# Optimization experiments

Measured on AMD Instinct MI355X. Metric: run time of the kernel, lower is better.

Reference implementation:

```python
import jax, jax.numpy as jnp
import numpy as np

B, A, V, D = 16, 1024, 1024, 512


def setup_inputs() -> dict:
    key = jax.random.key(0)
    k1, k2 = jax.random.split(key)
    audio_encoded = jax.random.normal(k1, (B, A, D), dtype=jnp.float32)
    visual_encoded = jax.random.normal(k2, (B, V, D), dtype=jnp.float32)
    return {"audio_encoded": audio_encoded, "visual_encoded": visual_encoded}


def reference(audio_encoded, visual_encoded):
    # Batched pairwise L2 distance: out[b, a, v] = ||audio[b,a] - visual[b,v]||_2
    # Fused ||a||^2 + ||v||^2 - 2 a.v formulation (single batched GEMM) replacing
    # the original per-(batch, audio-frame) Python loop of diff/pow/sum/sqrt.
    a_sq = jnp.sum(audio_encoded * audio_encoded, axis=-1)   # [B, A]
    v_sq = jnp.sum(visual_encoded * visual_encoded, axis=-1)  # [B, V]
    cross = jnp.einsum("bad,bvd->bav", audio_encoded, visual_encoded)  # [B, A, V]
    dist_sq = a_sq[:, :, None] + v_sq[:, None, :] - 2.0 * cross
    dist_sq = jnp.maximum(dist_sq, 0.0)  # clamp fp round-off negatives
    l2_features = jnp.sqrt(dist_sq)  # [B, A, V]
    return l2_features
```

## Files before the change

### kernel.cpp

```cpp
#include <hip/hip_runtime.h>
#include <hip/hip_bf16.h>

typedef __attribute__((ext_vector_type(8))) short short8;
typedef __attribute__((ext_vector_type(4))) float fv4;

constexpr int B_ = 16, A_ = 1024, V_ = 1024, D_ = 512;

__device__ __forceinline__ unsigned cvtpk(float lo, float hi) {
    unsigned r;
    asm("v_cvt_pk_bf16_f32 %0, %1, %2" : "=v"(r) : "v"(lo), "v"(hi));
    return r;
}
#define SB0() __builtin_amdgcn_sched_barrier(0)

struct Stage { fv4 x0, x1, x2, x3; };

__global__ void __launch_bounds__(512, 2)
l2dist_fused256(const float* __restrict__ audio, const float* __restrict__ visual,
                float* __restrict__ out)
{
    __shared__ __align__(16) char sA[2 * 256 * 128];
    __shared__ __align__(16) char sB[2 * 256 * 128];
    __shared__ float lnrm[512];

    const int t = threadIdx.x, lane = t & 63, w = t >> 6;
    const int wm = w >> 2, wn = w & 3;

    const int orig = blockIdx.x;
    const int wg   = (orig & 7) * 32 + (orig >> 3);
    const int b = wg >> 4, tile = wg & 15, ab = tile >> 2, vb = tile & 3;

    const float* Ag = audio  + ((size_t)b * A_ + ab * 256) * D_;
    const float* Vg = visual + ((size_t)b * V_ + vb * 256) * D_;

    const int rg  = t >> 2;
    const int lq  = t & 3;
    const int key = rg & 7;
    const int lqo = ((lq >> 1) << 4) + (lq & 1) * 8;

    const float* g0 = Ag + (size_t)rg * D_ + lq * 4;
    const float* g1 = Ag + (size_t)(128 + rg) * D_ + lq * 4;
    const float* g2 = Vg + (size_t)rg * D_ + lq * 4;
    const float* g3 = Vg + (size_t)(128 + rg) * D_ + lq * 4;

    const int oLo = rg * 128;
    const int oHi = (128 + rg) * 128;
    float* n0 = &lnrm[rg];
    float* n1 = &lnrm[128 + rg];
    float* n2 = &lnrm[256 + rg];
    float* n3 = &lnrm[384 + rg];

#define ISSUE(S, gbase, koff) do {                                   \
        const float* _p = (gbase) + (koff);                          \
        S.x0 = *(const fv4*)(_p);      S.x1 = *(const fv4*)(_p + 16);\
        S.x2 = *(const fv4*)(_p + 32); S.x3 = *(const fv4*)(_p + 48);\
    } while (0)

#define PROC(S, dst, rowoff, nrmp) do {                                          \
        float _s = S.x0[0]*S.x0[0] + S.x0[1]*S.x0[1] + S.x0[2]*S.x0[2] + S.x0[3]*S.x0[3] \
                 + S.x1[0]*S.x1[0] + S.x1[1]*S.x1[1] + S.x1[2]*S.x1[2] + S.x1[3]*S.x1[3] \
                 + S.x2[0]*S.x2[0] + S.x2[1]*S.x2[1] + S.x2[2]*S.x2[2] + S.x2[3]*S.x2[3] \
                 + S.x3[0]*S.x3[0] + S.x3[1]*S.x3[1] + S.x3[2]*S.x3[2] + S.x3[3]*S.x3[3];\
        char* _d = (dst) + (rowoff);                                             \
        { int2 _v; _v.x = (int)cvtpk(S.x0[0], S.x0[1]); _v.y = (int)cvtpk(S.x0[2], S.x0[3]); \
          *(int2*)(_d + ((((0 + (lq >> 1)) ^ key) << 4) + (lq & 1) * 8)) = _v; } \
        { int2 _v; _v.x = (int)cvtpk(S.x1[0], S.x1[1]); _v.y = (int)cvtpk(S.x1[2], S.x1[3]); \
          *(int2*)(_d + ((((2 + (lq >> 1)) ^ key) << 4) + (lq & 1) * 8)) = _v; } \
        { int2 _v; _v.x = (int)cvtpk(S.x2[0], S.x2[1]); _v.y = (int)cvtpk(S.x2[2], S.x2[3]); \
          *(int2*)(_d + ((((4 + (lq >> 1)) ^ key) << 4) + (lq & 1) * 8)) = _v; } \
        { int2 _v; _v.x = (int)cvtpk(S.x3[0], S.x3[1]); _v.y = (int)cvtpk(S.x3[2], S.x3[3]); \
          *(int2*)(_d + ((((6 + (lq >> 1)) ^ key) << 4) + (lq & 1) * 8)) = _v; } \
        _s += __shfl_xor(_s, 1, 64);                                             \
        _s += __shfl_xor(_s, 2, 64);                                             \
        if (lq == 0) *(nrmp) += _s;                                              \
    } while (0)

    lnrm[t] = 0.f;
    __syncthreads();
    {
        Stage q0, q1, q2, q3;
        ISSUE(q0, g0, 0); ISSUE(q1, g1, 0); SB0();
        PROC(q0, sA, oLo, n0);
        ISSUE(q2, g2, 0); SB0();
        PROC(q1, sA, oHi, n1);
        ISSUE(q3, g3, 0); SB0();
        PROC(q2, sB, oLo, n2);
        PROC(q3, sB, oHi, n3);
    }
    __syncthreads();

    fv4 acc[8][4];
#pragma unroll
    for (int m = 0; m < 8; ++m)
#pragma unroll
        for (int n = 0; n < 4; ++n) acc[m][n] = fv4{0.f, 0.f, 0.f, 0.f};

    const int frow = lane & 15, fg = lane >> 4, xk = frow & 7;
    const int cof0 = ((0 + fg) ^ xk) << 4;
    const int cof1 = ((4 + fg) ^ xk) << 4;

#pragma unroll 1
    for (int kt = 0; kt < 8; ++kt) {
        const int cur = kt & 1;
        char* dstA = sA + (cur ^ 1) * 32768;
        char* dstB = sB + (cur ^ 1) * 32768;
        const char* Ab = sA + cur * 32768 + (wm * 128 + frow) * 128;
        const char* Bb = sB + cur * 32768 + (wn * 64 + frow) * 128;
        const int koff = (kt + 1) * 64;
        const bool st = (kt < 7);

        Stage q0, q1, q2, q3;
        if (st) { ISSUE(q0, g0, koff); ISSUE(q1, g1, koff); SB0(); }

        short8 av[4][2];
        {
            short8 bv[2][2];
#pragma unroll
            for (int m = 0; m < 4; ++m) {
                av[m][0] = *(const short8*)(Ab + m * 2048 + cof0);
                av[m][1] = *(const short8*)(Ab + m * 2048 + cof1);
            }
#pragma unroll
            for (int n = 0; n < 2; ++n) {
                bv[n][0] = *(const short8*)(Bb + n * 2048 + cof0);
                bv[n][1] = *(const short8*)(Bb + n * 2048 + cof1);
            }
            __builtin_amdgcn_s_setprio(1);
#pragma unroll
            for (int k = 0; k < 2; ++k)
#pragma unroll
                for (int m = 0; m < 4; ++m)
#pragma unroll
                    for (int n = 0; n < 2; ++n)
                        acc[m][n] = __builtin_amdgcn_mfma_f32_16x16x32_bf16(av[m][k], bv[n][k], acc[m][n], 0, 0, 0);
            __builtin_amdgcn_s_setprio(0);
        }
        if (st) { PROC(q0, dstA, oLo, n0); ISSUE(q2, g2, koff); SB0(); }

        short8 bv2[2][2];
        {
#pragma unroll
            for (int n = 0; n < 2; ++n) {
                bv2[n][0] = *(const short8*)(Bb + (n + 2) * 2048 + cof0);
                bv2[n][1] = *(const short8*)(Bb + (n + 2) * 2048 + cof1);
            }
            __builtin_amdgcn_s_setprio(1);
#pragma unroll
            for (int k = 0; k < 2; ++k)
#pragma unroll
                for (int m = 0; m < 4; ++m)
#pragma unroll
                    for (int n = 0; n < 2; ++n)
                        acc[m][n + 2] = __builtin_amdgcn_mfma_f32_16x16x32_bf16(av[m][k], bv2[n][k], acc[m][n + 2], 0, 0, 0);
            __builtin_amdgcn_s_setprio(0);
        }
        if (st) { PROC(q1, dstA, oHi, n1); ISSUE(q3, g3, koff); SB0(); }

        {
#pragma unroll
            for (int m = 0; m < 4; ++m) {
                av[m][0] = *(const short8*)(Ab + (m + 4) * 2048 + cof0);
                av[m][1] = *(const short8*)(Ab + (m + 4) * 2048 + cof1);
            }
            __builtin_amdgcn_s_setprio(1);
#pragma unroll
            for (int k = 0; k < 2; ++k)
#pragma unroll
                for (int m = 0; m < 4; ++m)
#pragma unroll
                    for (int n = 0; n < 2; ++n)
                        acc[m + 4][n + 2] = __builtin_amdgcn_mfma_f32_16x16x32_bf16(av[m][k], bv2[n][k], acc[m + 4][n + 2], 0, 0, 0);
            __builtin_amdgcn_s_setprio(0);
        }
        if (st) PROC(q2, dstB, oLo, n2);

        {
            short8 bv[2][2];
#pragma unroll
            for (int n = 0; n < 2; ++n) {
                bv[n][0] = *(const short8*)(Bb + n * 2048 + cof0);
                bv[n][1] = *(const short8*)(Bb + n * 2048 + cof1);
            }
            __builtin_amdgcn_s_setprio(1);
#pragma unroll
            for (int k = 0; k < 2; ++k)
#pragma unroll
                for (int m = 0; m < 4; ++m)
#pragma unroll
                    for (int n = 0; n < 2; ++n)
                        acc[m + 4][n] = __builtin_amdgcn_mfma_f32_16x16x32_bf16(av[m][k], bv[n][k], acc[m + 4][n], 0, 0, 0);
            __builtin_amdgcn_s_setprio(0);
        }
        if (st) PROC(q3, dstB, oHi, n3);

        __syncthreads();
    }

    float* Ob = out + (size_t)b * A_ * V_ + (size_t)(ab * 256) * V_ + vb * 256;
#pragma unroll
    for (int m = 0; m < 8; ++m) {
#pragma unroll
        for (int n = 0; n < 4; ++n) {
            const int col = wn * 64 + n * 16 + frow;
            const float vsq = lnrm[256 + col];
#pragma unroll
            for (int j = 0; j < 4; ++j) {
                const int row = wm * 128 + m * 16 + fg * 4 + j;
                float d2 = lnrm[row] + vsq - 2.f * acc[m][n][j];
                Ob[(size_t)row * V_ + col] = sqrtf(fmaxf(d2, 0.f));
            }
        }
    }
#undef ISSUE
#undef PROC
}

extern "C" void kernel_launch(void* const* d_in, const int* in_sizes, int n_in,
                              void* d_out, int out_size, void* d_ws, size_t ws_size,
                              hipStream_t stream) {
    const float* audio  = (const float*)d_in[0];
    const float* visual = (const float*)d_in[1];
    float* out = (float*)d_out;
    l2dist_fused256<<<256, 512, 0, stream>>>(audio, visual, out);
}
```

Before: 41.10 us.

## Prefetch audio tiles one iteration earlier and accumulate norms in registers

Global loads for the first two A stages are now issued at the end of the previous iteration, before the barrier, so their latency overlaps the sync and the first MFMA block. The prologue issues all four stage loads at once. Row norms are kept as per-thread register partial sums and reduced with shuffles once after the main loop, which removes per-step shuffles and LDS read-modify-writes and the initial zeroing barrier. In exchange, register pressure rises because the q0/q1 stages stay live across the barrier, and an extra barrier is added before the epilogue.

New measurement: 49.17 us. 19.6% more time.

```diff
diff --git a/kernel.cpp b/kernel.cpp
--- a/kernel.cpp
+++ b/kernel.cpp
@@ -36,7 +36,6 @@
     const int rg  = t >> 2;
     const int lq  = t & 3;
     const int key = rg & 7;
-    const int lqo = ((lq >> 1) << 4) + (lq & 1) * 8;
 
     const float* g0 = Ag + (size_t)rg * D_ + lq * 4;
     const float* g1 = Ag + (size_t)(128 + rg) * D_ + lq * 4;
@@ -45,10 +44,8 @@
 
     const int oLo = rg * 128;
     const int oHi = (128 + rg) * 128;
-    float* n0 = &lnrm[rg];
-    float* n1 = &lnrm[128 + rg];
-    float* n2 = &lnrm[256 + rg];
-    float* n3 = &lnrm[384 + rg];
+
+    float ps0 = 0.f, ps1 = 0.f, ps2 = 0.f, ps3 = 0.f;
 
 #define ISSUE(S, gbase, koff) do {                                   \
         const float* _p = (gbase) + (koff);                          \
@@ -56,11 +53,11 @@
         S.x2 = *(const fv4*)(_p + 32); S.x3 = *(const fv4*)(_p + 48);\
     } while (0)
 
-#define PROC(S, dst, rowoff, nrmp) do {                                          \
-        float _s = S.x0[0]*S.x0[0] + S.x0[1]*S.x0[1] + S.x0[2]*S.x0[2] + S.x0[3]*S.x0[3] \
-                 + S.x1[0]*S.x1[0] + S.x1[1]*S.x1[1] + S.x1[2]*S.x1[2] + S.x1[3]*S.x1[3] \
-                 + S.x2[0]*S.x2[0] + S.x2[1]*S.x2[1] + S.x2[2]*S.x2[2] + S.x2[3]*S.x2[3] \
-                 + S.x3[0]*S.x3[0] + S.x3[1]*S.x3[1] + S.x3[2]*S.x3[2] + S.x3[3]*S.x3[3];\
+#define PROC(S, dst, rowoff, ps) do {                                            \
+        ps += S.x0[0]*S.x0[0] + S.x0[1]*S.x0[1] + S.x0[2]*S.x0[2] + S.x0[3]*S.x0[3] \
+            + S.x1[0]*S.x1[0] + S.x1[1]*S.x1[1] + S.x1[2]*S.x1[2] + S.x1[3]*S.x1[3] \
+            + S.x2[0]*S.x2[0] + S.x2[1]*S.x2[1] + S.x2[2]*S.x2[2] + S.x2[3]*S.x2[3] \
+            + S.x3[0]*S.x3[0] + S.x3[1]*S.x3[1] + S.x3[2]*S.x3[2] + S.x3[3]*S.x3[3];\
         char* _d = (dst) + (rowoff);                                             \
         { int2 _v; _v.x = (int)cvtpk(S.x0[0], S.x0[1]); _v.y = (int)cvtpk(S.x0[2], S.x0[3]); \
           *(int2*)(_d + ((((0 + (lq >> 1)) ^ key) << 4) + (lq & 1) * 8)) = _v; } \
@@ -70,23 +67,18 @@
           *(int2*)(_d + ((((4 + (lq >> 1)) ^ key) << 4) + (lq & 1) * 8)) = _v; } \
         { int2 _v; _v.x = (int)cvtpk(S.x3[0], S.x3[1]); _v.y = (int)cvtpk(S.x3[2], S.x3[3]); \
           *(int2*)(_d + ((((6 + (lq >> 1)) ^ key) << 4) + (lq & 1) * 8)) = _v; } \
-        _s += __shfl_xor(_s, 1, 64);                                             \
-        _s += __shfl_xor(_s, 2, 64);                                             \
-        if (lq == 0) *(nrmp) += _s;                                              \
     } while (0)
 
-    lnrm[t] = 0.f;
-    __syncthreads();
+    Stage q0, q1, q2, q3;
     {
-        Stage q0, q1, q2, q3;
-        ISSUE(q0, g0, 0); ISSUE(q1, g1, 0); SB0();
-        PROC(q0, sA, oLo, n0);
-        ISSUE(q2, g2, 0); SB0();
-        PROC(q1, sA, oHi, n1);
-        ISSUE(q3, g3, 0); SB0();
-        PROC(q2, sB, oLo, n2);
-        PROC(q3, sB, oHi, n3);
-    }
+        Stage p0, p1, p2, p3;
+        ISSUE(p0, g0, 0); ISSUE(p1, g1, 0); ISSUE(p2, g2, 0); ISSUE(p3, g3, 0); SB0();
+        PROC(p0, sA, oLo, ps0);
+        PROC(p1, sA, oHi, ps1);
+        PROC(p2, sB, oLo, ps2);
+        PROC(p3, sB, oHi, ps3);
+    }
+    ISSUE(q0, g0, 64); ISSUE(q1, g1, 64); SB0();
     __syncthreads();
 
     fv4 acc[8][4];
@@ -109,9 +101,6 @@
         const int koff = (kt + 1) * 64;
         const bool st = (kt < 7);
 
-        Stage q0, q1, q2, q3;
-        if (st) { ISSUE(q0, g0, koff); ISSUE(q1, g1, koff); SB0(); }
-
         short8 av[4][2];
         {
             short8 bv[2][2];
@@ -135,7 +124,7 @@
                         acc[m][n] = __builtin_amdgcn_mfma_f32_16x16x32_bf16(av[m][k], bv[n][k], acc[m][n], 0, 0, 0);
             __builtin_amdgcn_s_setprio(0);
         }
-        if (st) { PROC(q0, dstA, oLo, n0); ISSUE(q2, g2, koff); SB0(); }
+        if (st) { PROC(q0, dstA, oLo, ps0); ISSUE(q2, g2, koff); SB0(); }
 
         short8 bv2[2][2];
         {
@@ -154,7 +143,7 @@
                         acc[m][n + 2] = __builtin_amdgcn_mfma_f32_16x16x32_bf16(av[m][k], bv2[n][k], acc[m][n + 2], 0, 0, 0);
             __builtin_amdgcn_s_setprio(0);
         }
-        if (st) { PROC(q1, dstA, oHi, n1); ISSUE(q3, g3, koff); SB0(); }
+        if (st) { PROC(q1, dstA, oHi, ps1); ISSUE(q3, g3, koff); SB0(); }
 
         {
 #pragma unroll
@@ -172,7 +161,7 @@
                         acc[m + 4][n + 2] = __builtin_amdgcn_mfma_f32_16x16x32_bf16(av[m][k], bv2[n][k], acc[m + 4][n + 2], 0, 0, 0);
             __builtin_amdgcn_s_setprio(0);
         }
-        if (st) PROC(q2, dstB, oLo, n2);
+        if (st) PROC(q2, dstB, oLo, ps2);
 
         {
             short8 bv[2][2];
@@ -191,10 +180,27 @@
                         acc[m + 4][n] = __builtin_amdgcn_mfma_f32_16x16x32_bf16(av[m][k], bv[n][k], acc[m + 4][n], 0, 0, 0);
             __builtin_amdgcn_s_setprio(0);
         }
-        if (st) PROC(q3, dstB, oHi, n3);
+        if (st) PROC(q3, dstB, oHi, ps3);
+
+        if (kt < 6) {
+            const int koff2 = (kt + 2) * 64;
+            ISSUE(q0, g0, koff2); ISSUE(q1, g1, koff2); SB0();
+        }
 
         __syncthreads();
     }
+
+    ps0 += __shfl_xor(ps0, 1, 64); ps0 += __shfl_xor(ps0, 2, 64);
+    ps1 += __shfl_xor(ps1, 1, 64); ps1 += __shfl_xor(ps1, 2, 64);
+    ps2 += __shfl_xor(ps2, 1, 64); ps2 += __shfl_xor(ps2, 2, 64);
+    ps3 += __shfl_xor(ps3, 1, 64); ps3 += __shfl_xor(ps3, 2, 64);
+    if (lq == 0) {
+        lnrm[rg]       = ps0;
+        lnrm[128 + rg] = ps1;
+        lnrm[256 + rg] = ps2;
+        lnrm[384 + rg] = ps3;
+    }
+    __syncthreads();
 
     float* Ob = out + (size_t)b * A_ * V_ + (size_t)(ab * 256) * V_ + vb * 256;
 #pragma unroll
```
